# Optimization experiments

Measured on AMD Instinct MI355X. Metric: run time of the kernel, lower is better.

Reference implementation:

```python
import jax, jax.numpy as jnp
import numpy as np
from jax import lax

BOX = 64    # fixed box height/width (ymax-ymin == xmax-xmin == 64)
PROC = 128  # DetectionInputProcessor output size hardcoded in preprocessing


def _subnet(x, W):
    # stand-in for self._patch: 3x3 SAME conv (3->3) + tanh on a [H,W,3] crop
    y = lax.conv_general_dilated(x[None], W, (1, 1), 'SAME',
                                 dimension_numbers=('NHWC', 'HWIO', 'NHWC'))[0]
    return jnp.tanh(y)


def setup_inputs() -> dict:
    key = jax.random.key(0)
    k1, k2, k3 = jax.random.split(key, 3)
    B, H, Wd, N = 8, 1024, 1024, 8
    images = jax.random.uniform(k1, (B, H, Wd, 3), dtype=jnp.float32)  # in [0,1] subset of [-1,1]
    W = jax.random.normal(k2, (3, 3, 3, 3), dtype=jnp.float32) * 0.1
    box_yx = jax.random.randint(k3, (B, N, 2), 0, H - BOX, dtype=jnp.int32)
    return {"images": images, "W": W, "box_yx": box_yx}


def reference(images, W, box_yx):
    def per_image(image, yx):
        # sequential while_loop over boxes -> lax.scan (boxes may overlap)
        def body(carry, yx_i):
            img, loss = carry
            y, x = yx_i[0], yx_i[1]
            crop = lax.dynamic_slice(img, (y, x, 0), (BOX, BOX, 3))          # crop
            pb = jax.image.resize(crop, (PROC, PROC, 3), 'bilinear')          # preprocessing (resize to 128)
            im = _subnet(pb, W)                                               # self._patch call
            loss = loss + jnp.mean((im - pb) ** 2)                            # loss accumulation
            im2 = jax.image.resize(im, (BOX, BOX, 3), 'bilinear')             # postprocessing (resize back)
            img = lax.dynamic_update_slice(img, im2, (y, x, 0))               # tensor_scatter_nd_update
            img = jnp.clip(img, -1.0, 1.0)                                    # clip_by_value
            return (img, loss), None
        (img, loss), _ = lax.scan(body, (image, jnp.float32(0.0)), yx)
        return img, loss

    out_images, losses = jax.vmap(per_image)(images, box_yx)
    # map_fn returns the running (shared-variable) loss per image -> cumulative sum
    return out_images, jnp.cumsum(losses)
```

## Files before the change

### kernel.cpp

```cpp
#include <hip/hip_runtime.h>


#define PTHR 256
#define NPB 512

#define IMG_FLOATS (1024 * 1024 * 3)
#define IMG_BYTES ((size_t)8 * IMG_FLOATS * 4)
#define LOSS_OFF ((size_t)IMG_FLOATS * 8)

__device__ __forceinline__ int iclamp(int v, int lo, int hi) {
  return v < lo ? lo : (v > hi ? hi : v);
}
__device__ __forceinline__ float tanh_fast(float x) {
  float t = __expf(2.0f * x);
  return 1.0f - 2.0f / (t + 1.0f);
}

__global__ __launch_bounds__(128) void init_kernel(int* __restrict__ wsI) {
  wsI[threadIdx.x] = 0;
}

__global__ __launch_bounds__(PTHR, 2) void patch_kernel(
    const float* __restrict__ gin, const float* __restrict__ gW,
    const int* __restrict__ gbox, float* __restrict__ gout,
    int* __restrict__ wsI, float* __restrict__ wsLoss) {
  __shared__ float sCrop[12][193];
  __shared__ float sPlane[18][129];
  __shared__ float sWred[4];

  const int bid = blockIdx.x;
  const int tid = threadIdx.x;
  const int box = bid >> 3;
  const int band = bid & 7;
  const int img = box >> 3;
  const int k = box & 7;
  int* boxDone = wsI;

  int jy[8], jx[8];
#pragma unroll
  for (int j = 0; j < 8; ++j) {
    jy[j] = gbox[img * 16 + 2 * j];
    jx[j] = gbox[img * 16 + 2 * j + 1];
  }
  int y0 = 0, x0 = 0;
#pragma unroll
  for (int j = 0; j < 8; ++j)
    if (j == k) { y0 = jy[j]; x0 = jx[j]; }

  bool ov[8];
  bool hasPred = false, hasSucc = false;
#pragma unroll
  for (int j = 0; j < 8; ++j) {
    int dy = y0 - jy[j]; dy = dy < 0 ? -dy : dy;
    int dx = x0 - jx[j]; dx = dx < 0 ? -dx : dx;
    ov[j] = (dy < 64) && (dx < 64);
    hasPred = hasPred || (j < k && ov[j]);
    hasSucc = hasSucc || (j > k && ov[j]);
  }

  if (tid == 0 && hasPred) {
#pragma unroll
    for (int j = 0; j < 8; ++j) {
      if (j < k && ov[j]) {
        while (__hip_atomic_load(&boxDone[img * 8 + j], __ATOMIC_RELAXED,
                                 __HIP_MEMORY_SCOPE_AGENT) < 8) {
          __builtin_amdgcn_s_sleep(2);
        }
      }
    }
    __builtin_amdgcn_fence(__ATOMIC_ACQUIRE, "agent");
  }
  __syncthreads();

  const size_t ibase = (size_t)img * IMG_FLOATS;
  const int cropBase = 8 * band - 2;

#pragma unroll
  for (int q = 0; q < 3; ++q) {
    const int idx = tid + q * PTHR;
    const int r = idx >> 6, col = idx & 63;
    const int gr = iclamp(cropBase + r, 0, 63);
    const int gy = y0 + gr, gx = x0 + col;
    const float* src = gin;
    if (hasPred) {
      bool covered = false;
#pragma unroll
      for (int j = 0; j < 8; ++j) {
        bool cj = (j < k) && ((unsigned)(gy - jy[j]) < 64u) &&
                  ((unsigned)(gx - jx[j]) < 64u);
        covered = covered || cj;
      }
      if (covered) src = gout;
    }
    const size_t a = ibase + ((size_t)gy * 1024 + gx) * 3;
    sCrop[r][col * 3 + 0] = src[a + 0];
    sCrop[r][col * 3 + 1] = src[a + 1];
    sCrop[r][col * 3 + 2] = src[a + 2];
  }
  __syncthreads();

  const int m = tid >> 6, tx = tid & 63;
  const int r0 = 16 * band + 4 * m;
  const int hg = (tid < 128) ? 16 * band - 1 : 16 * band + 16;
  const int hh = iclamp(hg, 0, 127);
  const int hx = tid & 127;
  const int hslot = (tid < 128) ? 0 : 17;

  float lossAcc = 0.f;

#pragma unroll 1
  for (int c = 0; c < 3; ++c) {
    float wk[27];
#pragma unroll
    for (int t9 = 0; t9 < 9; ++t9)
#pragma unroll
      for (int ci = 0; ci < 3; ++ci) wk[ci * 9 + t9] = gW[(t9 * 3 + ci) * 3 + c];

    float acc[4][2];
#pragma unroll
    for (int p = 0; p < 4; ++p) { acc[p][0] = 0.f; acc[p][1] = 0.f; }
    float pbown[4][2];

#pragma unroll
    for (int ci = 0; ci < 3; ++ci) {
      float cv[4][3];
#pragma unroll
      for (int a = 0; a < 4; ++a)
#pragma unroll
        for (int b = 0; b < 3; ++b)
          cv[a][b] = sCrop[2 * m + 1 + a][iclamp(tx - 1 + b, 0, 63) * 3 + ci];
      float tmp[4][4];
#pragma unroll
      for (int a = 0; a < 4; ++a) {
        tmp[a][0] = 0.75f * cv[a][0] + 0.25f * cv[a][1];
        tmp[a][1] = 0.25f * cv[a][0] + 0.75f * cv[a][1];
        tmp[a][2] = 0.75f * cv[a][1] + 0.25f * cv[a][2];
        tmp[a][3] = 0.25f * cv[a][1] + 0.75f * cv[a][2];
      }
#pragma unroll
      for (int i = 0; i < 6; ++i) {
        float pr[4];
        const int a = i >> 1;
        const float w = (i & 1) ? 0.25f : 0.75f;
#pragma unroll
        for (int j = 0; j < 4; ++j)
          pr[j] = w * tmp[a][j] + (1.0f - w) * tmp[a + 1][j];
        if (i == 0 && r0 == 0) { pr[0] = pr[1] = pr[2] = pr[3] = 0.f; }
        if (i == 5 && r0 == 124) { pr[0] = pr[1] = pr[2] = pr[3] = 0.f; }
        if (tx == 0) pr[0] = 0.f;
        if (tx == 63) pr[3] = 0.f;
        if (ci == c && i >= 1 && i <= 4) {
          pbown[i - 1][0] = pr[1];
          pbown[i - 1][1] = pr[2];
        }
#pragma unroll
        for (int p = 0; p < 4; ++p) {
          const int du = i - p;
          if (du >= 0 && du < 3) {
#pragma unroll
            for (int dv = 0; dv < 3; ++dv) {
              const float wt = wk[ci * 9 + du * 3 + dv];
              acc[p][0] += wt * pr[dv];
              acc[p][1] += wt * pr[1 + dv];
            }
          }
        }
      }
    }
#pragma unroll
    for (int p = 0; p < 4; ++p)
#pragma unroll
      for (int q = 0; q < 2; ++q) {
        const float imv = tanh_fast(acc[p][q]);
        const float d = imv - pbown[p][q];
        lossAcc += d * d;
        sPlane[4 * m + p + 1][2 * tx + q] = imv;
      }

    float hacc = 0.f;
#pragma unroll
    for (int ci = 0; ci < 3; ++ci) {
#pragma unroll
      for (int du = 0; du < 3; ++du) {
        const int U = hh - 1 + du;
        if (U >= 0 && U < 128) {
          const int Lr = (U - 1) >> 1;
          const float wr = (U & 1) ? 0.75f : 0.25f;
          const int l0 = Lr - cropBase, l1 = l0 + 1;
#pragma unroll
          for (int dv = 0; dv < 3; ++dv) {
            const int V = hx - 1 + dv;
            if (V >= 0 && V < 128) {
              const int Lc = (V - 1) >> 1;
              const float wc = (V & 1) ? 0.75f : 0.25f;
              const int c0 = iclamp(Lc, 0, 63) * 3 + ci;
              const int c1 = iclamp(Lc + 1, 0, 63) * 3 + ci;
              const float v0 = wc * sCrop[l0][c0] + (1.0f - wc) * sCrop[l0][c1];
              const float v1 = wc * sCrop[l1][c0] + (1.0f - wc) * sCrop[l1][c1];
              hacc += wk[ci * 9 + du * 3 + dv] * (wr * v0 + (1.0f - wr) * v1);
            }
          }
        }
      }
    }
    sPlane[hslot][hx] = tanh_fast(hacc);
    __syncthreads();

    constexpr float W37 = 0.75f / 1.75f;
    constexpr float W17 = 0.25f / 1.75f;
    const int pbase = 16 * band - 1;
#pragma unroll
    for (int q2 = 0; q2 < 2; ++q2) {
      const int idx = tid + q2 * PTHR;
      const int Y = 8 * band + (idx >> 6), X = idx & 63;
      float wy[4] = {0.125f, 0.375f, 0.375f, 0.125f};
      float wx[4] = {0.125f, 0.375f, 0.375f, 0.125f};
      if (Y == 0) { wy[0] = 0.f; wy[1] = W37; wy[2] = W37; wy[3] = W17; }
      if (Y == 63) { wy[0] = W17; wy[1] = W37; wy[2] = W37; wy[3] = 0.f; }
      if (X == 0) { wx[0] = 0.f; wx[1] = W37; wx[2] = W37; wx[3] = W17; }
      if (X == 63) { wx[0] = W17; wx[1] = W37; wx[2] = W37; wx[3] = 0.f; }
      float sum = 0.f;
#pragma unroll
      for (int t2 = 0; t2 < 4; ++t2) {
        const int ryl = iclamp(2 * Y - 1 + t2, 0, 127) - pbase;
        float rs = 0.f;
#pragma unroll
        for (int u = 0; u < 4; ++u)
          rs += wx[u] * sPlane[ryl][iclamp(2 * X - 1 + u, 0, 127)];
        sum += wy[t2] * rs;
      }
      gout[ibase + ((size_t)(y0 + Y) * 1024 + (x0 + X)) * 3 + c] = sum;
    }
    __syncthreads();
  }

#pragma unroll
  for (int mm = 32; mm >= 1; mm >>= 1) lossAcc += __shfl_xor(lossAcc, mm, 64);
  if ((tid & 63) == 0) sWred[tid >> 6] = lossAcc;
  __syncthreads();
  if (tid == 0)
    wsLoss[bid] = sWred[0] + sWred[1] + sWred[2] + sWred[3];

  if (hasSucc) {
    __syncthreads();
    if (tid == 0) {
      __threadfence();
      __hip_atomic_fetch_add(&boxDone[img * 8 + k], 1, __ATOMIC_RELEASE,
                             __HIP_MEMORY_SCOPE_AGENT);
    }
  }
}

__global__ __launch_bounds__(64) void finalize_kernel(
    const float* __restrict__ wsLoss, float* __restrict__ gout) {
  __shared__ float simg[8];
  const int t = threadIdx.x;
  if (t < 8) {
    float s = 0.f;
    for (int i = 0; i < 64; ++i) s += wsLoss[t * 64 + i];
    simg[t] = s / 49152.0f;
  }
  __syncthreads();
  if (t == 0) {
    float run = 0.f;
#pragma unroll
    for (int im = 0; im < 8; ++im) {
      run += simg[im];
      gout[LOSS_OFF + im] = run;
    }
  }
}

extern "C" void kernel_launch(void* const* d_in, const int* in_sizes, int n_in,
                              void* d_out, int out_size, void* d_ws, size_t ws_size,
                              hipStream_t stream) {
  (void)in_sizes; (void)n_in; (void)out_size; (void)ws_size;
  const float* gin = (const float*)d_in[0];
  const float* gW = (const float*)d_in[1];
  const int* gbox = (const int*)d_in[2];
  float* gout = (float*)d_out;
  int* wsI = (int*)d_ws;
  float* wsLoss = (float*)d_ws + 128;

  hipLaunchKernelGGL(init_kernel, dim3(1), dim3(128), 0, stream, wsI);
  (void)hipMemcpyAsync(gout, gin, IMG_BYTES, hipMemcpyDeviceToDevice, stream);
  hipLaunchKernelGGL(patch_kernel, dim3(NPB), dim3(PTHR), 0, stream,
                     gin, gW, gbox, gout, wsI, wsLoss);
  hipLaunchKernelGGL(finalize_kernel, dim3(1), dim3(64), 0, stream,
                     wsLoss, gout);
}
```

Baseline: 74.89 us.

## Fuse image copy into patch kernel and skip box-covered regions

Drops the separate device-to-device memcpy of all images and adds 2048 extra copy blocks to the patch kernel. Each copy block moves 4 rows with vectorized nontemporal stores and skips the floats inside any box, which the patch blocks write. This removes a separate copy operation, overlaps the copy with the patch work, and avoids writing the same box pixels twice. In exchange there is per-element overlap-test logic, scalar stores on box edges, and reliance on the patch blocks fully covering every box region so nothing is left unwritten.

```diff
diff --git a/kernel.cpp b/kernel.cpp
--- a/kernel.cpp
+++ b/kernel.cpp
@@ -3,10 +3,13 @@
 
 #define PTHR 256
 #define NPB 512
+#define NCOPY 2048
+#define NBLK (NPB + NCOPY)
 
 #define IMG_FLOATS (1024 * 1024 * 3)
-#define IMG_BYTES ((size_t)8 * IMG_FLOATS * 4)
 #define LOSS_OFF ((size_t)IMG_FLOATS * 8)
+
+typedef float f32x4 __attribute__((ext_vector_type(4)));
 
 __device__ __forceinline__ int iclamp(int v, int lo, int hi) {
   return v < lo ? lo : (v > hi ? hi : v);
@@ -20,7 +23,7 @@
   wsI[threadIdx.x] = 0;
 }
 
-__global__ __launch_bounds__(PTHR, 2) void patch_kernel(
+__global__ __launch_bounds__(PTHR, 2) void fused_kernel(
     const float* __restrict__ gin, const float* __restrict__ gW,
     const int* __restrict__ gbox, float* __restrict__ gout,
     int* __restrict__ wsI, float* __restrict__ wsLoss) {
@@ -30,6 +33,67 @@
 
   const int bid = blockIdx.x;
   const int tid = threadIdx.x;
+
+  if (bid >= NPB) {
+    const int cid = bid - NPB;
+    const int img = cid >> 8;
+    const int row0 = (cid & 255) * 4;
+    const size_t fbase = (size_t)cid * 12288;
+
+    int by[8], bs[8];
+#pragma unroll
+    for (int j = 0; j < 8; ++j) {
+      by[j] = gbox[img * 16 + 2 * j];
+      bs[j] = gbox[img * 16 + 2 * j + 1] * 3;
+    }
+    bool anyRow = false;
+#pragma unroll
+    for (int j = 0; j < 8; ++j)
+      anyRow = anyRow || ((by[j] < row0 + 4) && (row0 < by[j] + 64));
+
+    const f32x4* src = (const f32x4*)(gin + fbase);
+    f32x4* dst = (f32x4*)(gout + fbase);
+    f32x4 v[12];
+#pragma unroll
+    for (int q = 0; q < 12; ++q) v[q] = src[tid + q * PTHR];
+
+    if (!anyRow) {
+#pragma unroll
+      for (int q = 0; q < 12; ++q)
+        __builtin_nontemporal_store(v[q], &dst[tid + q * PTHR]);
+    } else {
+#pragma unroll
+      for (int q = 0; q < 12; ++q) {
+        const int c = tid + q * PTHR;
+        const int r = c / 768;
+        const int xf = (c - r * 768) * 4;
+        const int y = row0 + r;
+        bool anyOv = false, fullIn = false;
+#pragma unroll
+        for (int j = 0; j < 8; ++j) {
+          const bool rowHit = (unsigned)(y - by[j]) < 64u;
+          anyOv = anyOv || (rowHit && (xf + 4 > bs[j]) && (xf < bs[j] + 192));
+          fullIn = fullIn || (rowHit && (xf >= bs[j]) && (xf + 4 <= bs[j] + 192));
+        }
+        if (!anyOv) {
+          __builtin_nontemporal_store(v[q], &dst[tid + q * PTHR]);
+        } else if (!fullIn) {
+#pragma unroll
+          for (int i = 0; i < 4; ++i) {
+            const int xfi = xf + i;
+            bool inside = false;
+#pragma unroll
+            for (int j = 0; j < 8; ++j)
+              inside = inside || (((unsigned)(y - by[j]) < 64u) &&
+                                  (xfi >= bs[j]) && (xfi < bs[j] + 192));
+            if (!inside) gout[fbase + (size_t)c * 4 + i] = v[q][i];
+          }
+        }
+      }
+    }
+    return;
+  }
+
   const int box = bid >> 3;
   const int band = bid & 7;
   const int img = box >> 3;
@@ -283,8 +347,7 @@
   float* wsLoss = (float*)d_ws + 128;
 
   hipLaunchKernelGGL(init_kernel, dim3(1), dim3(128), 0, stream, wsI);
-  (void)hipMemcpyAsync(gout, gin, IMG_BYTES, hipMemcpyDeviceToDevice, stream);
-  hipLaunchKernelGGL(patch_kernel, dim3(NPB), dim3(PTHR), 0, stream,
+  hipLaunchKernelGGL(fused_kernel, dim3(NBLK), dim3(PTHR), 0, stream,
                      gin, gW, gbox, gout, wsI, wsLoss);
   hipLaunchKernelGGL(finalize_kernel, dim3(1), dim3(64), 0, stream,
                      wsLoss, gout);
```

Result: faster. 67.48 us (-9.9%).
